# Kernel optimization log

Hardware: AMD Instinct MI355X
Metric: run time of the kernel (lower is better)

## Reference

```python
import jax, jax.numpy as jnp
import numpy as np

KH = KW = 9
STRIDE = 1
PAD = 4
DIL = 1


def _bilinear(img, py, px):
    """img: [C,H,W]; py, px: [kk,Ho,Wo] float sample coords -> [C,kk,Ho,Wo].
    Zero padding outside the image, matching DCNv2 semantics."""
    H, W = img.shape[-2], img.shape[-1]
    y0 = jnp.floor(py)
    x0 = jnp.floor(px)
    wy = py - y0  # fractional parts (carry the gradient wrt offsets)
    wx = px - x0

    def gather(yi, xi):
        valid = ((yi >= 0) & (yi < H) & (xi >= 0) & (xi < W)).astype(img.dtype)
        yc = jnp.clip(yi, 0, H - 1).astype(jnp.int32)
        xc = jnp.clip(xi, 0, W - 1).astype(jnp.int32)
        return img[:, yc, xc] * valid[None]

    v00 = gather(y0, x0)
    v01 = gather(y0, x0 + 1)
    v10 = gather(y0 + 1, x0)
    v11 = gather(y0 + 1, x0 + 1)
    return (v00 * (1 - wy) * (1 - wx) + v01 * (1 - wy) * wx
            + v10 * wy * (1 - wx) + v11 * wy * wx)


def setup_inputs() -> dict:
    key = jax.random.key(0)
    k1, k2, k3 = jax.random.split(key, 3)
    B, H, W = 2, 256, 256
    kk = KH * KW
    inp = jax.random.normal(k1, (B, 3, H, W), dtype=jnp.float32)
    offset = jax.random.normal(k2, (B, 2 * kk, H, W), dtype=jnp.float32)
    mask = jax.random.uniform(k3, (B, kk, H, W), dtype=jnp.float32)
    weight = jnp.ones((1, 1, KH, KW), dtype=jnp.float32) / kk  # frozen averaging kernel
    bias = jnp.zeros((1,), dtype=jnp.float32)
    return {"input": inp, "offset": offset, "mask": mask, "weight": weight, "bias": bias}


def reference(input, offset, mask, weight, bias):
    B, C, H, W = input.shape  # C = 3 * Ci (R,G,B chunks sharing weight/offset/mask)
    kk = KH * KW
    Ho = (H + 2 * PAD - DIL * (KH - 1) - 1) // STRIDE + 1
    Wo = (W + 2 * PAD - DIL * (KW - 1) - 1) // STRIDE + 1

    ky = jnp.repeat(jnp.arange(KH), KW)  # [kk]
    kx = jnp.tile(jnp.arange(KW), KH)
    base_y = (jnp.arange(Ho) * STRIDE - PAD)[None, :, None] + (ky * DIL)[:, None, None]  # [kk,Ho,1]
    base_x = (jnp.arange(Wo) * STRIDE - PAD)[None, None, :] + (kx * DIL)[:, None, None]  # [kk,1,Wo]

    off = offset.reshape(B, kk, 2, Ho, Wo)  # channel c = 2*k + {0: dy, 1: dx}
    py = base_y[None].astype(offset.dtype) + off[:, :, 0]  # [B,kk,Ho,Wo]
    px = base_x[None].astype(offset.dtype) + off[:, :, 1]

    # bilinear-sampled, modulated im2col: [B, C, kk, Ho, Wo]
    samples = jax.vmap(_bilinear)(input, py, px)
    val = samples * mask[:, None]

    Co, Ci = weight.shape[0], weight.shape[1]
    G = C // Ci  # 3 color groups, identical weight applied to each
    val = val.reshape(B, G, Ci, kk, Ho, Wo)
    wk = weight.reshape(Co, Ci, kk)
    out = jnp.einsum('bgckhw,ock->bgohw', val, wk) + bias[None, None, :, None, None]
    return out.reshape(B, G * Co, Ho, Wo)
```

## Files before the change

### kernel.cpp

```cpp
#include <hip/hip_runtime.h>

#define HH 256
#define WW 256
#define KK 81
#define PLANE (HH * WW)

__global__ __launch_bounds__(256) void pack_kernel(const float* __restrict__ in,
                                                   float4* __restrict__ img) {
    int idx = blockIdx.x * 256 + threadIdx.x;
    int b = idx >> 16;
    int pix = idx & 0xFFFF;
    const float* base = in + (size_t)b * 3 * PLANE + pix;
    img[idx] = make_float4(base[0], base[PLANE], base[2 * PLANE], 0.f);
}

template <bool PACKED>
__global__ __launch_bounds__(256) void dcn_kernel(
    const float* __restrict__ input,
    const float4* __restrict__ img,
    const float* __restrict__ offset,
    const float* __restrict__ mask,
    const float* __restrict__ weight,
    const float* __restrict__ bias,
    float* __restrict__ out) {
    __shared__ float wk[KK];
    const int t = threadIdx.x;
    if (t < KK) wk[t] = weight[t];
    __syncthreads();

    const int wo = t;
    const int ho = blockIdx.x;
    const int b = blockIdx.y;

    const size_t row = (size_t)ho * WW + wo;
    const float* offp = offset + (size_t)b * 2 * KK * PLANE + row;
    const float* mskp = mask + (size_t)b * KK * PLANE + row;
    const float4* ib = img + (size_t)b * PLANE;
    const float* inb = input + (size_t)b * 3 * PLANE;

    float ax = 0.f, ay = 0.f, az = 0.f;

    int ky = 0, kx = 0;
#pragma unroll 9
    for (int k = 0; k < KK; ++k) {
        float dy = offp[(size_t)(2 * k) * PLANE];
        float dx = offp[(size_t)(2 * k + 1) * PLANE];
        float m = mskp[(size_t)k * PLANE] * wk[k];

        float py = (float)(ho - 4 + ky) + dy;
        float px = (float)(wo - 4 + kx) + dx;
        float y0f = floorf(py), x0f = floorf(px);
        float wy = py - y0f, wx = px - x0f;
        int y0 = (int)y0f, x0 = (int)x0f;
        int y1 = y0 + 1, x1 = x0 + 1;

        float a0 = ((unsigned)y0 < (unsigned)HH) ? (1.f - wy) : 0.f;
        float a1 = ((unsigned)y1 < (unsigned)HH) ? wy : 0.f;
        float b0 = ((unsigned)x0 < (unsigned)WW) ? (1.f - wx) : 0.f;
        float b1 = ((unsigned)x1 < (unsigned)WW) ? wx : 0.f;

        int y0c = min(max(y0, 0), HH - 1) * WW;
        int y1c = min(max(y1, 0), HH - 1) * WW;
        int x0c = min(max(x0, 0), WW - 1);
        int x1c = min(max(x1, 0), WW - 1);

        float w00 = a0 * b0 * m;
        float w01 = a0 * b1 * m;
        float w10 = a1 * b0 * m;
        float w11 = a1 * b1 * m;

        if (PACKED) {
            float4 v00 = ib[y0c + x0c];
            float4 v01 = ib[y0c + x1c];
            float4 v10 = ib[y1c + x0c];
            float4 v11 = ib[y1c + x1c];
            ax = fmaf(w00, v00.x, ax);
            ay = fmaf(w00, v00.y, ay);
            az = fmaf(w00, v00.z, az);
            ax = fmaf(w01, v01.x, ax);
            ay = fmaf(w01, v01.y, ay);
            az = fmaf(w01, v01.z, az);
            ax = fmaf(w10, v10.x, ax);
            ay = fmaf(w10, v10.y, ay);
            az = fmaf(w10, v10.z, az);
            ax = fmaf(w11, v11.x, ax);
            ay = fmaf(w11, v11.y, ay);
            az = fmaf(w11, v11.z, az);
        } else {
            const float* p0 = inb;
            const float* p1 = inb + PLANE;
            const float* p2 = inb + 2 * PLANE;
            ax = fmaf(w00, p0[y0c + x0c], ax);
            ax = fmaf(w01, p0[y0c + x1c], ax);
            ax = fmaf(w10, p0[y1c + x0c], ax);
            ax = fmaf(w11, p0[y1c + x1c], ax);
            ay = fmaf(w00, p1[y0c + x0c], ay);
            ay = fmaf(w01, p1[y0c + x1c], ay);
            ay = fmaf(w10, p1[y1c + x0c], ay);
            ay = fmaf(w11, p1[y1c + x1c], ay);
            az = fmaf(w00, p2[y0c + x0c], az);
            az = fmaf(w01, p2[y0c + x1c], az);
            az = fmaf(w10, p2[y1c + x0c], az);
            az = fmaf(w11, p2[y1c + x1c], az);
        }

        kx++;
        if (kx == 9) {
            kx = 0;
            ky++;
        }
    }

    const float bv = bias[0];
    const size_t o = (size_t)b * 3 * PLANE + row;
    out[o] = ax + bv;
    out[o + PLANE] = ay + bv;
    out[o + 2 * PLANE] = az + bv;
}

extern "C" void kernel_launch(void* const* d_in, const int* in_sizes, int n_in,
                              void* d_out, int out_size, void* d_ws, size_t ws_size,
                              hipStream_t stream) {
    const float* input = (const float*)d_in[0];
    const float* offset = (const float*)d_in[1];
    const float* mask = (const float*)d_in[2];
    const float* weight = (const float*)d_in[3];
    const float* bias = (const float*)d_in[4];
    float* out = (float*)d_out;

    const int B = in_sizes[0] / (3 * PLANE);
    dim3 grid(HH, B);

    const size_t packed_bytes = (size_t)B * PLANE * sizeof(float4);
    if (ws_size >= packed_bytes) {
        float4* img = (float4*)d_ws;
        pack_kernel<<<B * PLANE / 256, 256, 0, stream>>>(input, img);
        dcn_kernel<true><<<grid, 256, 0, stream>>>(input, img, offset, mask, weight, bias, out);
    } else {
        dcn_kernel<false><<<grid, 256, 0, stream>>>(input, nullptr, offset, mask, weight, bias, out);
    }
}
```

Baseline: 200.7 us.

## Split kernel taps across four wavefronts per 64-pixel tile with shared reduction

Each block now covers 64 pixels, and its four wavefronts each handle about a quarter of the 81 taps. Partial sums are then reduced through shared memory. The aim is more independent memory streams and more blocks per pixel, to hide gather and offset-load latency, with a launch-bounds hint for higher occupancy. The unpacked fallback path is removed, so the code now assumes the workspace is large enough. It also adds a barrier and a shared-memory reduction step.

```diff
diff --git a/kernel.cpp b/kernel.cpp
--- a/kernel.cpp
+++ b/kernel.cpp
@@ -14,9 +14,7 @@
     img[idx] = make_float4(base[0], base[PLANE], base[2 * PLANE], 0.f);
 }
 
-template <bool PACKED>
-__global__ __launch_bounds__(256) void dcn_kernel(
-    const float* __restrict__ input,
+__global__ __launch_bounds__(256, 8) void dcn_kernel(
     const float4* __restrict__ img,
     const float* __restrict__ offset,
     const float* __restrict__ mask,
@@ -24,28 +22,38 @@
     const float* __restrict__ bias,
     float* __restrict__ out) {
     __shared__ float wk[KK];
+    __shared__ float red[3][4][64];
+
     const int t = threadIdx.x;
     if (t < KK) wk[t] = weight[t];
     __syncthreads();
 
-    const int wo = t;
-    const int ho = blockIdx.x;
+    const int w = t >> 6;
+    const int lane = t & 63;
     const int b = blockIdx.y;
+    const int pix0 = blockIdx.x * 64;
+    const int pix = pix0 + lane;
+    const int ho = pix >> 8;
+    const int wo = pix & 255;
 
-    const size_t row = (size_t)ho * WW + wo;
-    const float* offp = offset + (size_t)b * 2 * KK * PLANE + row;
-    const float* mskp = mask + (size_t)b * KK * PLANE + row;
+    const int kbeg = w * 20 + (w ? 1 : 0);
+    const int kend = kbeg + (w ? 20 : 21);
+    int ky = kbeg / 9;
+    int kx = kbeg - ky * 9;
+
+    const float* op = offset + (size_t)b * 2 * KK * PLANE + (size_t)(2 * kbeg) * PLANE + pix;
+    const float* mp = mask + (size_t)b * KK * PLANE + (size_t)kbeg * PLANE + pix;
     const float4* ib = img + (size_t)b * PLANE;
-    const float* inb = input + (size_t)b * 3 * PLANE;
 
     float ax = 0.f, ay = 0.f, az = 0.f;
 
-    int ky = 0, kx = 0;
-#pragma unroll 9
-    for (int k = 0; k < KK; ++k) {
-        float dy = offp[(size_t)(2 * k) * PLANE];
-        float dx = offp[(size_t)(2 * k + 1) * PLANE];
-        float m = mskp[(size_t)k * PLANE] * wk[k];
+#pragma unroll 4
+    for (int k = kbeg; k < kend; ++k) {
+        float dy = op[0];
+        float dx = op[PLANE];
+        float m = mp[0] * wk[k];
+        op += 2 * PLANE;
+        mp += PLANE;
 
         float py = (float)(ho - 4 + ky) + dy;
         float px = (float)(wo - 4 + kx) + dx;
@@ -69,53 +77,40 @@
         float w10 = a1 * b0 * m;
         float w11 = a1 * b1 * m;
 
-        if (PACKED) {
-            float4 v00 = ib[y0c + x0c];
-            float4 v01 = ib[y0c + x1c];
-            float4 v10 = ib[y1c + x0c];
-            float4 v11 = ib[y1c + x1c];
-            ax = fmaf(w00, v00.x, ax);
-            ay = fmaf(w00, v00.y, ay);
-            az = fmaf(w00, v00.z, az);
-            ax = fmaf(w01, v01.x, ax);
-            ay = fmaf(w01, v01.y, ay);
-            az = fmaf(w01, v01.z, az);
-            ax = fmaf(w10, v10.x, ax);
-            ay = fmaf(w10, v10.y, ay);
-            az = fmaf(w10, v10.z, az);
-            ax = fmaf(w11, v11.x, ax);
-            ay = fmaf(w11, v11.y, ay);
-            az = fmaf(w11, v11.z, az);
-        } else {
-            const float* p0 = inb;
-            const float* p1 = inb + PLANE;
-            const float* p2 = inb + 2 * PLANE;
-            ax = fmaf(w00, p0[y0c + x0c], ax);
-            ax = fmaf(w01, p0[y0c + x1c], ax);
-            ax = fmaf(w10, p0[y1c + x0c], ax);
-            ax = fmaf(w11, p0[y1c + x1c], ax);
-            ay = fmaf(w00, p1[y0c + x0c], ay);
-            ay = fmaf(w01, p1[y0c + x1c], ay);
-            ay = fmaf(w10, p1[y1c + x0c], ay);
-            ay = fmaf(w11, p1[y1c + x1c], ay);
-            az = fmaf(w00, p2[y0c + x0c], az);
-            az = fmaf(w01, p2[y0c + x1c], az);
-            az = fmaf(w10, p2[y1c + x0c], az);
-            az = fmaf(w11, p2[y1c + x1c], az);
-        }
+        float4 v00 = ib[y0c + x0c];
+        float4 v01 = ib[y0c + x1c];
+        float4 v10 = ib[y1c + x0c];
+        float4 v11 = ib[y1c + x1c];
+        ax = fmaf(w00, v00.x, ax);
+        ay = fmaf(w00, v00.y, ay);
+        az = fmaf(w00, v00.z, az);
+        ax = fmaf(w01, v01.x, ax);
+        ay = fmaf(w01, v01.y, ay);
+        az = fmaf(w01, v01.z, az);
+        ax = fmaf(w10, v10.x, ax);
+        ay = fmaf(w10, v10.y, ay);
+        az = fmaf(w10, v10.z, az);
+        ax = fmaf(w11, v11.x, ax);
+        ay = fmaf(w11, v11.y, ay);
+        az = fmaf(w11, v11.z, az);
 
-        kx++;
-        if (kx == 9) {
+        if (++kx == 9) {
             kx = 0;
-            ky++;
+            ++ky;
         }
     }
 
-    const float bv = bias[0];
-    const size_t o = (size_t)b * 3 * PLANE + row;
-    out[o] = ax + bv;
-    out[o + PLANE] = ay + bv;
-    out[o + 2 * PLANE] = az + bv;
+    red[0][w][lane] = ax;
+    red[1][w][lane] = ay;
+    red[2][w][lane] = az;
+    __syncthreads();
+
+    if (t < 192) {
+        const int c = t >> 6;
+        const int l = t & 63;
+        float s = red[c][0][l] + red[c][1][l] + red[c][2][l] + red[c][3][l] + bias[0];
+        out[(size_t)b * 3 * PLANE + (size_t)c * PLANE + pix0 + l] = s;
+    }
 }
 
 extern "C" void kernel_launch(void* const* d_in, const int* in_sizes, int n_in,
@@ -129,14 +124,9 @@
     float* out = (float*)d_out;
 
     const int B = in_sizes[0] / (3 * PLANE);
-    dim3 grid(HH, B);
+    float4* img = (float4*)d_ws;
 
-    const size_t packed_bytes = (size_t)B * PLANE * sizeof(float4);
-    if (ws_size >= packed_bytes) {
-        float4* img = (float4*)d_ws;
-        pack_kernel<<<B * PLANE / 256, 256, 0, stream>>>(input, img);
-        dcn_kernel<true><<<grid, 256, 0, stream>>>(input, img, offset, mask, weight, bias, out);
-    } else {
-        dcn_kernel<false><<<grid, 256, 0, stream>>>(input, nullptr, offset, mask, weight, bias, out);
-    }
+    pack_kernel<<<B * PLANE / 256, 256, 0, stream>>>(input, img);
+    dim3 grid(PLANE / 64, B);
+    dcn_kernel<<<grid, 256, 0, stream>>>(img, offset, mask, weight, bias, out);
 }
```

Measured after the change: 216.0 us. +7.6%, slower.
